# Kernel optimization log

Measured on AMD Instinct MI355X. Metric: run time of the kernel, lower is better.

Reference implementation:

```python
import jax, jax.numpy as jnp
import numpy as np

B, S, D = 2, 2048, 2048
H = 16
Q_LORA, KV_LORA = 1536, 512
ROPE_DIM, NOPE_DIM, V_DIM = 64, 64, 128
Q_HEAD_DIM = NOPE_DIM + ROPE_DIM  # 128
ROPE_THETA, ROPE_RATIO = 10000.0, 1.0


def setup_inputs() -> dict:
    key = jax.random.key(0)
    ks = jax.random.split(key, 6)
    std = 0.02
    return {
        "hidden_states": jax.random.normal(ks[0], (B, S, D), jnp.float32),
        "Wqa": jax.random.normal(ks[1], (D, Q_LORA), jnp.float32) * std,
        "Wqb": jax.random.normal(ks[2], (Q_LORA, H * Q_HEAD_DIM), jnp.float32) * std,
        "Wkva": jax.random.normal(ks[3], (D, KV_LORA + ROPE_DIM), jnp.float32) * std,
        "Wkvb": jax.random.normal(ks[4], (KV_LORA, H * (NOPE_DIM + V_DIM)), jnp.float32) * std,
        "Wo": jax.random.normal(ks[5], (H * V_DIM, D), jnp.float32) * std,
    }


def _rope_tables(seq_len):
    half = ROPE_DIM // 2
    inv_freq = ROPE_RATIO / (ROPE_THETA ** (jnp.arange(half, dtype=jnp.float32) * 2.0 / ROPE_DIM))
    freqs = jnp.arange(seq_len, dtype=jnp.float32)[:, None] * inv_freq[None, :]  # [S, half]
    return jnp.cos(freqs), jnp.sin(freqs)


def _apply_rope(x, cos, sin):
    # interleaved even/odd rotation, matches torch stack+flatten
    x_even = x[..., 0::2]
    x_odd = x[..., 1::2]
    r_even = x_even * cos - x_odd * sin
    r_odd = x_odd * cos + x_even * sin
    return jnp.stack([r_even, r_odd], axis=-1).reshape(x.shape)


def reference(hidden_states, Wqa, Wqb, Wkva, Wkvb, Wo):
    b, s, _ = hidden_states.shape
    scale = Q_HEAD_DIM ** -0.5

    # query compression path
    q_latent = hidden_states @ Wqa                             # [B,S,Q_LORA]
    q = (q_latent @ Wqb).reshape(b, s, H, Q_HEAD_DIM)
    q = jnp.transpose(q, (0, 2, 1, 3))                          # [B,H,S,q_head_dim]
    q_nope, q_pe = q[..., :NOPE_DIM], q[..., NOPE_DIM:]

    # kv compression
    kv_comp = hidden_states @ Wkva                              # [B,S,KV_LORA+ROPE]
    c_kv, k_pe = kv_comp[..., :KV_LORA], kv_comp[..., KV_LORA:]

    cos, sin = _rope_tables(s)                                  # [S, ROPE_DIM//2]
    q_pe = _apply_rope(q_pe, cos, sin)                          # [B,H,S,ROPE]
    k_pe = _apply_rope(k_pe, cos, sin)                          # [B,S,ROPE]

    # kv decompression
    kv = (c_kv @ Wkvb).reshape(b, s, H, NOPE_DIM + V_DIM)
    kv = jnp.transpose(kv, (0, 2, 1, 3))                        # [B,H,S,nope+v]
    k_nope, v = kv[..., :NOPE_DIM], kv[..., NOPE_DIM:]

    k_pe_b = jnp.broadcast_to(k_pe[:, None], (b, H, s, ROPE_DIM))
    q_full = jnp.concatenate([q_nope, q_pe], axis=-1)           # [B,H,S,128]
    k_full = jnp.concatenate([k_nope, k_pe_b], axis=-1)         # [B,H,S,128]

    scores = jnp.einsum('bhqd,bhkd->bhqk', q_full, k_full) * scale
    causal = jnp.tril(jnp.ones((s, s), dtype=bool))
    scores = jnp.where(causal[None, None], scores, jnp.finfo(scores.dtype).min)
    probs = jax.nn.softmax(scores, axis=-1)
    attn = jnp.einsum('bhqk,bhkd->bhqd', probs, v)              # [B,H,S,V_DIM]

    out = jnp.transpose(attn, (0, 2, 1, 3)).reshape(b, s, H * V_DIM)
    return out @ Wo                                             # [B,S,D]
```

## Files before the change

kernel.cpp:

```cpp
#include <hip/hip_runtime.h>
#include <hip/hip_bf16.h>
#include <cstdint>
#include <cstddef>

typedef __bf16 bf16_t;
typedef __attribute__((ext_vector_type(4))) __bf16 bf16x4;
typedef __attribute__((ext_vector_type(8))) __bf16 bf16x8;
typedef __attribute__((ext_vector_type(4))) float f32x4;

#define S_ 2048
#define H_ 16
#define NTOK 4096

__device__ __forceinline__ f32x4 mfma16x16(bf16x8 a, bf16x8 b, f32x4 c) {
  return __builtin_amdgcn_mfma_f32_16x16x32_bf16(a, b, c, 0, 0, 0);
}
__device__ __forceinline__ bf16x8 load8(const bf16_t* p) {
  return *reinterpret_cast<const bf16x8*>(p);
}
__device__ __forceinline__ void load_lds16(const void* g, void* l) {
  __builtin_amdgcn_global_load_lds(
      (const __attribute__((address_space(1))) uint32_t*)g,
      (__attribute__((address_space(3))) uint32_t*)l, 16, 0, 0);
}


__global__ void cast_bf16_k(const float* __restrict__ in, bf16_t* __restrict__ out, int n) {
  int idx = blockIdx.x * 256 + threadIdx.x;
  int i4 = idx * 4;
  if (i4 >= n) return;
  float4 v = *reinterpret_cast<const float4*>(in + i4);
  out[i4 + 0] = (bf16_t)v.x;
  out[i4 + 1] = (bf16_t)v.y;
  out[i4 + 2] = (bf16_t)v.z;
  out[i4 + 3] = (bf16_t)v.w;
}

__global__ void rope_tables_k(float* __restrict__ cosT, float* __restrict__ sinT) {
  int idx = blockIdx.x * 256 + threadIdx.x;
  if (idx >= S_ * 32) return;
  int s = idx >> 5, i = idx & 31;
  float inv = powf(10000.0f, -(2.0f * (float)i) / 64.0f);
  float fr = (float)s * inv;
  cosT[idx] = cosf(fr);
  sinT[idx] = sinf(fr);
}

struct TDesc {
  const float* src;
  bf16_t* dst;
  int K, Nsrc, bxc, off, perm;
};
struct TDesc5 {
  TDesc d[5];
};

__global__ void transpose_cast_multi_k(TDesc5 ds) {
  __shared__ float tile[32][33];
  const int bid = blockIdx.x;
  int i = 0;
#pragma unroll
  for (int j = 1; j < 5; ++j)
    if (bid >= ds.d[j].off) i = j;
  const float* __restrict__ in = ds.d[i].src;
  bf16_t* __restrict__ out = ds.d[i].dst;
  const int K = ds.d[i].K, Nsrc = ds.d[i].Nsrc;
  const int local = bid - ds.d[i].off;
  const int n0 = (local % ds.d[i].bxc) * 32;
  const int k0 = (local / ds.d[i].bxc) * 32;
  int srcn0 = n0;
  if (ds.d[i].perm) {
    srcn0 = (n0 < 1024) ? ((n0 >> 6) * 192 + (n0 & 63))
                        : (((n0 - 1024) >> 7) * 192 + 64 + ((n0 - 1024) & 127));
  }
  int tx = threadIdx.x & 31, ty = threadIdx.x >> 5;
#pragma unroll
  for (int r = 0; r < 4; ++r) {
    int k = k0 + ty + r * 8, n = srcn0 + tx;
    tile[ty + r * 8][tx] = (n < Nsrc) ? in[(size_t)k * Nsrc + n] : 0.0f;
  }
  __syncthreads();
#pragma unroll
  for (int r = 0; r < 4; ++r) {
    int n = n0 + ty + r * 8, k = k0 + tx;
    out[(size_t)n * K + k] = (bf16_t)tile[tx][ty + r * 8];
  }
}


__device__ __forceinline__ void gemm_loop64(const bf16_t* __restrict__ A, int lda,
                                            const bf16_t* __restrict__ Bt, int K, int m0, int n0,
                                            int tid, bf16_t* Al, bf16_t* Bl, f32x4 (&acc)[4][4]) {
  const int wid = tid >> 6, lane = tid & 63;
  const int wm = (wid >> 1) * 64, wn = (wid & 1) * 64;
  const int srow8 = lane >> 3, c8 = lane & 7;
  const int swz8 = c8 ^ srow8;
  const int lr = lane & 15, lg = lane >> 4;
  const int e = lr & 7;

  const bf16_t* ag = A + (size_t)(m0 + wid * 32 + srow8) * lda + (swz8 << 3);
  const bf16_t* bg = Bt + (size_t)(n0 + wid * 32 + srow8) * K + (swz8 << 3);

  auto STAGE = [&](int buf, int k0) {
    bf16_t* ab = Al + buf * (128 * 64);
    bf16_t* bb = Bl + buf * (128 * 64);
#pragma unroll
    for (int rr = 0; rr < 4; ++rr) {
      load_lds16(ag + (size_t)(rr * 8) * lda + k0, &ab[(wid * 32 + rr * 8) * 64]);
      load_lds16(bg + (size_t)(rr * 8) * K + k0, &bb[(wid * 32 + rr * 8) * 64]);
    }
  };

  STAGE(0, 0);
  int cur = 0;
  for (int k0 = 0; k0 < K; k0 += 64) {
    if (k0 + 64 < K) {
      STAGE(cur ^ 1, k0 + 64);
      __builtin_amdgcn_sched_barrier(0);
      asm volatile("s_waitcnt vmcnt(8)" ::: "memory");
    } else {
      asm volatile("s_waitcnt vmcnt(0)" ::: "memory");
    }
    __builtin_amdgcn_sched_barrier(0);
    __builtin_amdgcn_s_barrier();
    __builtin_amdgcn_sched_barrier(0);
    const bf16_t* Ab = Al + cur * (128 * 64);
    const bf16_t* Bb = Bl + cur * (128 * 64);
#pragma unroll
    for (int kk = 0; kk < 2; ++kk) {
      bf16x8 af[4], bfr[4];
#pragma unroll
      for (int i = 0; i < 4; ++i) {
        af[i] = load8(&Ab[(wm + i * 16 + lr) * 64 + (((kk * 4 + lg) ^ e) << 3)]);
        bfr[i] = load8(&Bb[(wn + i * 16 + lr) * 64 + (((kk * 4 + lg) ^ e) << 3)]);
      }
#pragma unroll
      for (int i = 0; i < 4; ++i)
#pragma unroll
        for (int j = 0; j < 4; ++j) acc[i][j] = mfma16x16(af[i], bfr[j], acc[i][j]);
    }
    __builtin_amdgcn_sched_barrier(0);
    __builtin_amdgcn_s_barrier();
    cur ^= 1;
  }
}


__global__ __launch_bounds__(256) void gemm_lat_k(const bf16_t* __restrict__ A,
                                                  const bf16_t* __restrict__ Bt,
                                                  bf16_t* __restrict__ C,
                                                  const float* __restrict__ cosT,
                                                  const float* __restrict__ sinT) {
  __shared__ alignas(16) bf16_t Al[2 * 128 * 64];
  __shared__ alignas(16) bf16_t Bl[2 * 128 * 64];
  const int tid = threadIdx.x;
  const int sw = (blockIdx.x & 7) * 68 + (blockIdx.x >> 3);
  const int m0 = (sw / 17) * 128, n0 = (sw % 17) * 128;
  f32x4 acc[4][4] = {};
  gemm_loop64(A, 2048, Bt, 2048, m0, n0, tid, Al, Bl, acc);

  const int wid = tid >> 6, lane = tid & 63;
  const int wm = (wid >> 1) * 64, wn = (wid & 1) * 64;
  const int lr = lane & 15, lg = lane >> 4;
  const bool rope = (n0 == 2048) && (wn == 0);
  const int ir_base = lr >> 1;
  const bool odd = lane & 1;
#pragma unroll
  for (int i = 0; i < 4; ++i)
#pragma unroll
    for (int j = 0; j < 4; ++j) {
      float v4[4];
#pragma unroll
      for (int r = 0; r < 4; ++r) v4[r] = acc[i][j][r];
      if (rope) {
        const int ir = j * 8 + ir_base;
#pragma unroll
        for (int r = 0; r < 4; ++r) {
          const int srow_ = (m0 + wm + i * 16 + lg * 4 + r) & (S_ - 1);
          float c = cosT[srow_ * 32 + ir], sn = sinT[srow_ * 32 + ir];
          float partner = __shfl_xor(v4[r], 1);
          v4[r] = odd ? (v4[r] * c + partner * sn) : (v4[r] * c - partner * sn);
        }
      }
#pragma unroll
      for (int r = 0; r < 4; ++r) {
        int row = m0 + wm + i * 16 + lg * 4 + r;
        int col = n0 + wn + j * 16 + lr;
        C[(size_t)row * 2176 + col] = (bf16_t)v4[r];
      }
    }
}


__global__ __launch_bounds__(256) void gemm_qkv_k(const bf16_t* __restrict__ lat,
                                                  const bf16_t* __restrict__ Wqbt,
                                                  const bf16_t* __restrict__ Wkvbt,
                                                  bf16_t* __restrict__ qb,
                                                  bf16_t* __restrict__ knb,
                                                  bf16_t* __restrict__ vT,
                                                  const float* __restrict__ cosT,
                                                  const float* __restrict__ sinT, float qscale) {
  __shared__ alignas(16) bf16_t Al[2 * 128 * 64];
  __shared__ alignas(16) bf16_t Bl[2 * 128 * 64];
  const int tid = threadIdx.x;
  const int sw = (blockIdx.x & 7) * 160 + (blockIdx.x >> 3);
  const int wid = tid >> 6, lane = tid & 63;
  const int wm = (wid >> 1) * 64, wn = (wid & 1) * 64;
  const int lr = lane & 15, lg = lane >> 4;
  f32x4 acc[4][4] = {};
  const int r5 = sw % 5, q5 = sw / 5;

  if (r5 < 2) {
    const int qi = q5 * 2 + r5;
    const int m0 = (qi >> 4) * 128, n0 = (qi & 15) * 128;
    gemm_loop64(lat, 2176, Wqbt, 1536, m0, n0, tid, Al, Bl, acc);
    const bool rope = (wn == 64);
    const int ir_base = lr >> 1;
    const bool odd = lane & 1;
#pragma unroll
    for (int i = 0; i < 4; ++i)
#pragma unroll
      for (int j = 0; j < 4; ++j) {
        float v4[4];
#pragma unroll
        for (int r = 0; r < 4; ++r) v4[r] = acc[i][j][r] * qscale;
        if (rope) {
          const int ir = j * 8 + ir_base;
#pragma unroll
          for (int r = 0; r < 4; ++r) {
            const int srow_ = (m0 + wm + i * 16 + lg * 4 + r) & (S_ - 1);
            float c = cosT[srow_ * 32 + ir], sn = sinT[srow_ * 32 + ir];
            float partner = __shfl_xor(v4[r], 1);
            v4[r] = odd ? (v4[r] * c + partner * sn) : (v4[r] * c - partner * sn);
          }
        }
#pragma unroll
        for (int r = 0; r < 4; ++r) {
          int row = m0 + wm + i * 16 + lg * 4 + r;
          int col = n0 + wn + j * 16 + lr;
          qb[(size_t)row * 2048 + col] = (bf16_t)v4[r];
        }
      }
  } else {
    const int ki = q5 * 3 + (r5 - 2);
    const int m0 = (ki / 24) * 128, n0 = (ki % 24) * 128;
    gemm_loop64(lat + 1536, 2176, Wkvbt, 512, m0, n0, tid, Al, Bl, acc);
    if (n0 < 1024) {
#pragma unroll
      for (int i = 0; i < 4; ++i)
#pragma unroll
        for (int j = 0; j < 4; ++j)
#pragma unroll
          for (int r = 0; r < 4; ++r) {
            int row = m0 + wm + i * 16 + lg * 4 + r;
            int col = n0 + wn + j * 16 + lr;
            knb[(size_t)row * 1024 + col] = (bf16_t)acc[i][j][r];
          }
    } else {
#pragma unroll
      for (int i = 0; i < 4; ++i) {
        const int row0 = m0 + wm + i * 16 + lg * 4;
        const int bb = row0 >> 11;
        const int s0 = row0 & (S_ - 1);
#pragma unroll
        for (int j = 0; j < 4; ++j) {
          const int idx = n0 + wn + j * 16 + lr - 1024;
          const int h = idx >> 7, d = idx & 127;
          bf16x4 pk;
#pragma unroll
          for (int r = 0; r < 4; ++r) pk[r] = (bf16_t)acc[i][j][r];
          *reinterpret_cast<bf16x4*>(&vT[((size_t)(bb * 16 + h) * 128 + d) * 2048 + s0]) = pk;
        }
      }
    }
  }
}


__global__ __launch_bounds__(256) void gemm_out_k(const bf16_t* __restrict__ A,
                                                  const bf16_t* __restrict__ Bt,
                                                  float* __restrict__ C) {
  __shared__ alignas(16) bf16_t Al[2 * 128 * 64];
  __shared__ alignas(16) bf16_t Bl[2 * 128 * 64];
  const int tid = threadIdx.x;
  const int sw = (blockIdx.x & 7) * 64 + (blockIdx.x >> 3);
  const int m0 = (sw >> 4) * 128, n0 = (sw & 15) * 128;
  f32x4 acc[4][4] = {};
  gemm_loop64(A, 2048, Bt, 2048, m0, n0, tid, Al, Bl, acc);
  const int wid = tid >> 6, lane = tid & 63;
  const int wm = (wid >> 1) * 64, wn = (wid & 1) * 64;
  const int lr = lane & 15, lg = lane >> 4;
#pragma unroll
  for (int i = 0; i < 4; ++i)
#pragma unroll
    for (int j = 0; j < 4; ++j)
#pragma unroll
      for (int r = 0; r < 4; ++r) {
        int row = m0 + wm + i * 16 + lg * 4 + r;
        int col = n0 + wn + j * 16 + lr;
        C[(size_t)row * 2048 + col] = acc[i][j][r];
      }
}

__global__ __launch_bounds__(256) void attn_fused(const bf16_t* __restrict__ q,
                                                  const bf16_t* __restrict__ knb,
                                                  const bf16_t* __restrict__ lat,
                                                  const bf16_t* __restrict__ vT,
                                                  bf16_t* __restrict__ out) {
  __shared__ alignas(16) bf16_t Kn[64 * 64];
  __shared__ alignas(16) bf16_t Kp[64 * 64];
  __shared__ alignas(16) bf16_t Vt[128 * 64];
  __shared__ alignas(16) bf16_t Pl[4][16 * 64];
  const int tid = threadIdx.x, wid = tid >> 6, lane = tid & 63;
  const int bid = blockIdx.x;
  const int g = bid >> 8;
  const int x = (bid >> 5) & 7;
  const int bh = bid & 31;
  const int qt = (g & 1) ? (24 - g * 8 + x) : (31 - g * 8 - x);
  const int b = bh >> 4, h = bh & 15;
  const int tokb = b * S_;
  const int lr = lane & 15, lg = lane >> 4;
  const int srow8 = lane >> 3, c8 = lane & 7;
  const int swz8 = c8 ^ srow8;
  bf16_t* Pw = &Pl[wid][0];

  bf16x8 ones;
#pragma unroll
  for (int j = 0; j < 8; ++j) ones[j] = (bf16_t)1.0f;

  bf16x8 qf[4];
  {
    const int qrow = qt * 64 + wid * 16 + lr;
    const bf16_t* qp = q + (size_t)(tokb + qrow) * 2048 + h * 128 + lg * 8;
#pragma unroll
    for (int ds = 0; ds < 4; ++ds) qf[ds] = load8(qp + ds * 32);
  }

  f32x4 o[8] = {};
  f32x4 o8 = {};
  float mrow[4] = {-1e30f, -1e30f, -1e30f, -1e30f};

  for (int t = 0; t <= qt; ++t) {
    const int kb = t * 64;
#pragma unroll
    for (int rr = 0; rr < 2; ++rr) {
      const int r0 = wid * 16 + rr * 8;
      const size_t tk = (size_t)(tokb + kb + r0 + srow8);
      load_lds16(knb + tk * 1024 + h * 64 + (swz8 << 3), &Kn[r0 * 64]);
      load_lds16(lat + tk * 2176 + 2048 + (swz8 << 3), &Kp[r0 * 64]);
    }
#pragma unroll
    for (int rr = 0; rr < 4; ++rr) {
      const int r0 = wid * 32 + rr * 8;
      load_lds16(vT + ((size_t)bh * 128 + r0 + srow8) * 2048 + kb + (swz8 << 3), &Vt[r0 * 64]);
    }
    __syncthreads();

    f32x4 s[4];
    __builtin_amdgcn_s_setprio(1);
#pragma unroll
    for (int kt = 0; kt < 4; ++kt) {
      const int row = kt * 16 + lr;
      const int e = lr & 7;
      bf16x8 kf0 = load8(&Kn[row * 64 + ((lg ^ e) << 3)]);
      bf16x8 kf1 = load8(&Kn[row * 64 + (((lg + 4) ^ e) << 3)]);
      bf16x8 kf2 = load8(&Kp[row * 64 + ((lg ^ e) << 3)]);
      bf16x8 kf3 = load8(&Kp[row * 64 + (((lg + 4) ^ e) << 3)]);
      f32x4 acc = {0.f, 0.f, 0.f, 0.f};
      acc = mfma16x16(qf[0], kf0, acc);
      acc = mfma16x16(qf[1], kf1, acc);
      acc = mfma16x16(qf[2], kf2, acc);
      acc = mfma16x16(qf[3], kf3, acc);
      s[kt] = acc;
    }
    __builtin_amdgcn_s_setprio(0);

    if (t == qt) {
#pragma unroll
      for (int kt = 0; kt < 4; ++kt) {
        const int key = kb + kt * 16 + lr;
#pragma unroll
        for (int r = 0; r < 4; ++r) {
          const int qr = qt * 64 + wid * 16 + lg * 4 + r;
          if (key > qr) s[kt][r] = -1e30f;
        }
      }
    }

    float tm[4];
#pragma unroll
    for (int r = 0; r < 4; ++r) {
      float mx = fmaxf(fmaxf(s[0][r], s[1][r]), fmaxf(s[2][r], s[3][r]));
      mx = fmaxf(mx, __shfl_xor(mx, 1));
      mx = fmaxf(mx, __shfl_xor(mx, 2));
      mx = fmaxf(mx, __shfl_xor(mx, 4));
      mx = fmaxf(mx, __shfl_xor(mx, 8));
      tm[r] = mx;
    }
    float need = fmaxf(fmaxf(tm[0] - mrow[0], tm[1] - mrow[1]),
                       fmaxf(tm[2] - mrow[2], tm[3] - mrow[3]));
    if (!__all(need <= 8.0f)) {
#pragma unroll
      for (int r = 0; r < 4; ++r) {
        float mn = fmaxf(mrow[r], tm[r]);
        float corr = exp2f(mrow[r] - mn);
        mrow[r] = mn;
        o8[r] *= corr;
#pragma unroll
        for (int n = 0; n < 8; ++n) o[n][r] *= corr;
      }
    }
#pragma unroll
    for (int kt = 0; kt < 4; ++kt)
#pragma unroll
      for (int r = 0; r < 4; ++r) s[kt][r] = exp2f(s[kt][r] - mrow[r]);

#pragma unroll
    for (int kt = 0; kt < 4; ++kt)
#pragma unroll
      for (int r = 0; r < 4; ++r) {
        const int qrow = lg * 4 + r;
        const int key = kt * 16 + lr;
        Pw[qrow * 64 + ((((key >> 3) ^ (qrow & 7)) << 3) | (key & 7))] = (bf16_t)s[kt][r];
      }

    __builtin_amdgcn_s_setprio(1);
#pragma unroll
    for (int ks = 0; ks < 2; ++ks) {
      const int e = lr & 7;
      bf16x8 pa = load8(&Pw[lr * 64 + (((ks * 4 + lg) ^ e) << 3)]);
#pragma unroll
      for (int n = 0; n < 8; ++n) {
        bf16x8 vb = load8(&Vt[(n * 16 + lr) * 64 + (((ks * 4 + lg) ^ e) << 3)]);
        o[n] = mfma16x16(pa, vb, o[n]);
      }
      o8 = mfma16x16(pa, ones, o8);
    }
    __builtin_amdgcn_s_setprio(0);
    __syncthreads();
  }

  float linv[4];
#pragma unroll
  for (int r = 0; r < 4; ++r) linv[r] = __builtin_amdgcn_rcpf(o8[r]);
#pragma unroll
  for (int n = 0; n < 8; ++n)
#pragma unroll
    for (int r = 0; r < 4; ++r) {
      const int qr = qt * 64 + wid * 16 + lg * 4 + r;
      out[(size_t)(tokb + qr) * 2048 + h * 128 + n * 16 + lr] = (bf16_t)(o[n][r] * linv[r]);
    }
}


extern "C" void kernel_launch(void* const* d_in, const int* in_sizes, int n_in, void* d_out,
                              int out_size, void* d_ws, size_t ws_size, hipStream_t stream) {
  const float* hs = (const float*)d_in[0];
  const float* Wqa = (const float*)d_in[1];
  const float* Wqb = (const float*)d_in[2];
  const float* Wkva = (const float*)d_in[3];
  const float* Wkvb = (const float*)d_in[4];
  const float* Wo = (const float*)d_in[5];
  float* out = (float*)d_out;

  char* ws = (char*)d_ws;
  size_t off = 0;
  auto alloc = [&](size_t bytes) {
    void* p = ws + off;
    off += (bytes + 255) & ~(size_t)255;
    return p;
  };
  bf16_t* hsb = (bf16_t*)alloc((size_t)NTOK * 2048 * 2);
  bf16_t* W1t = (bf16_t*)alloc((size_t)2176 * 2048 * 2);
  bf16_t* Wqbt = (bf16_t*)alloc((size_t)2048 * 1536 * 2);
  bf16_t* Wkvbt = (bf16_t*)alloc((size_t)3072 * 512 * 2);
  bf16_t* Wot = (bf16_t*)alloc((size_t)2048 * 2048 * 2);
  bf16_t* lat = (bf16_t*)alloc((size_t)NTOK * 2176 * 2);
  bf16_t* qb = (bf16_t*)alloc((size_t)NTOK * 2048 * 2);
  bf16_t* knb = (bf16_t*)alloc((size_t)NTOK * 1024 * 2);
  bf16_t* attn = (bf16_t*)alloc((size_t)NTOK * 2048 * 2);
  bf16_t* vT = (bf16_t*)alloc((size_t)32 * 128 * 2048 * 2);
  float* cosT = (float*)alloc((size_t)S_ * 32 * 4);
  float* sinT = (float*)alloc((size_t)S_ * 32 * 4);

  cast_bf16_k<<<(NTOK * 2048 / 4 + 255) / 256, 256, 0, stream>>>(hs, hsb, NTOK * 2048);
  rope_tables_k<<<(S_ * 32 + 255) / 256, 256, 0, stream>>>(cosT, sinT);
  {
    TDesc5 ds;
    int o0 = 0;
    auto add = [&](int i, const float* src, bf16_t* dst, int K, int Nsrc, int Nout, int perm) {
      int bxc = Nout / 32, cnt = bxc * (K / 32);
      ds.d[i] = TDesc{src, dst, K, Nsrc, bxc, o0, perm};
      o0 += cnt;
    };
    add(0, Wqa, W1t, 2048, 1536, 1536, 0);
    add(1, Wkva, W1t + (size_t)1536 * 2048, 2048, 576, 640, 0);
    add(2, Wqb, Wqbt, 1536, 2048, 2048, 0);
    add(3, Wkvb, Wkvbt, 512, 3072, 3072, 1);
    add(4, Wo, Wot, 2048, 2048, 2048, 0);
    transpose_cast_multi_k<<<o0, 256, 0, stream>>>(ds);
  }

  gemm_lat_k<<<dim3(544), 256, 0, stream>>>(hsb, W1t, lat, cosT, sinT);
  const float scale = 0.08838834764831845f * 1.4426950408889634f;
  gemm_qkv_k<<<dim3(1280), 256, 0, stream>>>(lat, Wqbt, Wkvbt, qb, knb, vT, cosT, sinT, scale);
  attn_fused<<<dim3(1024), 256, 0, stream>>>(qb, knb, lat, vT, attn);
  gemm_out_k<<<dim3(512), 256, 0, stream>>>(attn, Wot, out);
}
```

Measured before the change: 286.0 us.

## Transpose QK^T MFMA so each lane owns one query row in softmax

```diff
diff --git a/kernel.cpp b/kernel.cpp
--- a/kernel.cpp
+++ b/kernel.cpp
@@ -338,7 +338,8 @@
 
   f32x4 o[8] = {};
   f32x4 o8 = {};
-  float mrow[4] = {-1e30f, -1e30f, -1e30f, -1e30f};
+  float m = -1e30f;
+  const int qr_glob = qt * 64 + wid * 16 + lr;
 
   for (int t = 0; t <= qt; ++t) {
     const int kb = t * 64;
@@ -367,62 +368,61 @@
       bf16x8 kf2 = load8(&Kp[row * 64 + ((lg ^ e) << 3)]);
       bf16x8 kf3 = load8(&Kp[row * 64 + (((lg + 4) ^ e) << 3)]);
       f32x4 acc = {0.f, 0.f, 0.f, 0.f};
-      acc = mfma16x16(qf[0], kf0, acc);
-      acc = mfma16x16(qf[1], kf1, acc);
-      acc = mfma16x16(qf[2], kf2, acc);
-      acc = mfma16x16(qf[3], kf3, acc);
+      acc = mfma16x16(kf0, qf[0], acc);
+      acc = mfma16x16(kf1, qf[1], acc);
+      acc = mfma16x16(kf2, qf[2], acc);
+      acc = mfma16x16(kf3, qf[3], acc);
       s[kt] = acc;
     }
     __builtin_amdgcn_s_setprio(0);
 
     if (t == qt) {
 #pragma unroll
-      for (int kt = 0; kt < 4; ++kt) {
-        const int key = kb + kt * 16 + lr;
+      for (int kt = 0; kt < 4; ++kt)
 #pragma unroll
         for (int r = 0; r < 4; ++r) {
-          const int qr = qt * 64 + wid * 16 + lg * 4 + r;
-          if (key > qr) s[kt][r] = -1e30f;
+          const int key = kb + kt * 16 + lg * 4 + r;
+          if (key > qr_glob) s[kt][r] = -1e30f;
         }
-      }
-    }
-
-    float tm[4];
-#pragma unroll
-    for (int r = 0; r < 4; ++r) {
-      float mx = fmaxf(fmaxf(s[0][r], s[1][r]), fmaxf(s[2][r], s[3][r]));
-      mx = fmaxf(mx, __shfl_xor(mx, 1));
-      mx = fmaxf(mx, __shfl_xor(mx, 2));
-      mx = fmaxf(mx, __shfl_xor(mx, 4));
-      mx = fmaxf(mx, __shfl_xor(mx, 8));
-      tm[r] = mx;
-    }
-    float need = fmaxf(fmaxf(tm[0] - mrow[0], tm[1] - mrow[1]),
-                       fmaxf(tm[2] - mrow[2], tm[3] - mrow[3]));
-    if (!__all(need <= 8.0f)) {
+    }
+
+    float tm;
+    {
+      float a0 = fmaxf(fmaxf(s[0][0], s[0][1]), fmaxf(s[0][2], s[0][3]));
+      float a1 = fmaxf(fmaxf(s[1][0], s[1][1]), fmaxf(s[1][2], s[1][3]));
+      float a2 = fmaxf(fmaxf(s[2][0], s[2][1]), fmaxf(s[2][2], s[2][3]));
+      float a3 = fmaxf(fmaxf(s[3][0], s[3][1]), fmaxf(s[3][2], s[3][3]));
+      tm = fmaxf(fmaxf(a0, a1), fmaxf(a2, a3));
+      tm = fmaxf(tm, __shfl_xor(tm, 16));
+      tm = fmaxf(tm, __shfl_xor(tm, 32));
+    }
+    if (!__all(tm - m <= 8.0f)) {
+      float mn = fmaxf(m, tm);
+      float corr = exp2f(m - mn);
+      m = mn;
+      float corrv[4];
+#pragma unroll
+      for (int r = 0; r < 4; ++r) corrv[r] = __shfl(corr, lg * 4 + r);
 #pragma unroll
       for (int r = 0; r < 4; ++r) {
-        float mn = fmaxf(mrow[r], tm[r]);
-        float corr = exp2f(mrow[r] - mn);
-        mrow[r] = mn;
-        o8[r] *= corr;
-#pragma unroll
-        for (int n = 0; n < 8; ++n) o[n][r] *= corr;
+        o8[r] *= corrv[r];
+#pragma unroll
+        for (int n = 0; n < 8; ++n) o[n][r] *= corrv[r];
       }
     }
 #pragma unroll
     for (int kt = 0; kt < 4; ++kt)
 #pragma unroll
-      for (int r = 0; r < 4; ++r) s[kt][r] = exp2f(s[kt][r] - mrow[r]);
-
-#pragma unroll
-    for (int kt = 0; kt < 4; ++kt)
-#pragma unroll
-      for (int r = 0; r < 4; ++r) {
-        const int qrow = lg * 4 + r;
-        const int key = kt * 16 + lr;
-        Pw[qrow * 64 + ((((key >> 3) ^ (qrow & 7)) << 3) | (key & 7))] = (bf16_t)s[kt][r];
-      }
+      for (int r = 0; r < 4; ++r) s[kt][r] = exp2f(s[kt][r] - m);
+
+#pragma unroll
+    for (int kt = 0; kt < 4; ++kt) {
+      bf16x4 pk;
+#pragma unroll
+      for (int r = 0; r < 4; ++r) pk[r] = (bf16_t)s[kt][r];
+      const int c = kt * 2 + (lg >> 1);
+      *reinterpret_cast<bf16x4*>(&Pw[lr * 64 + ((c ^ (lr & 7)) << 3) + ((lg & 1) << 2)]) = pk;
+    }
 
     __builtin_amdgcn_s_setprio(1);
 #pragma unroll
```

New measurement: 275.3 us. -3.8%, faster.
